# Kernel tuning notes

Measured on AMD Instinct MI355X. Metric: run time of the kernel, lower is better.

## Reference

```python
import jax, jax.numpy as jnp
import numpy as np

EPS_LA = 1e-8
BN_EPS = 1e-5


def setup_inputs() -> dict:
    N, IN_C, HID, OUT_C = 8192, 64, 64, 32
    key = jax.random.key(0)
    ks = jax.random.split(key, 8)
    X = jax.random.normal(ks[0], (N, IN_C), dtype=jnp.float32)
    La = jax.random.uniform(ks[1], (N,), dtype=jnp.float32)  # eigenvalues in [0,1)
    U = jax.random.normal(ks[2], (N, N), dtype=jnp.float32)  # eigenvector matrix
    # learnable params
    ve = jnp.array([7.0], dtype=jnp.float32)   # Velocity(7)
    ve2 = jnp.array([0.0], dtype=jnp.float32)  # Velocity(0)
    W_w = jax.random.normal(ks[3], (HID, IN_C), dtype=jnp.float32) / np.sqrt(IN_C)
    W_b = jnp.zeros((HID,), dtype=jnp.float32)
    bn_gamma = jnp.ones((HID,), dtype=jnp.float32)
    bn_beta = jnp.zeros((HID,), dtype=jnp.float32)
    mlp_w = jax.random.normal(ks[4], (OUT_C, HID), dtype=jnp.float32) / np.sqrt(HID)
    mlp_b = jnp.zeros((OUT_C,), dtype=jnp.float32)
    return {"X": X, "La": La, "U": U, "ve": ve, "ve2": ve2,
            "W_w": W_w, "W_b": W_b, "bn_gamma": bn_gamma, "bn_beta": bn_beta,
            "mlp_w": mlp_w, "mlp_b": mlp_b}


def reference(X, La, U, ve, ve2, W_w, W_b, bn_gamma, bn_beta, mlp_w, mlp_b):
    # Spectral filter eigenvalue scalings (Velocity modules: elementwise pow)
    V_La = jnp.power(La, ve[0])                                # [N]
    V_La2 = jnp.power((2.0 * (La - EPS_LA) - 1.0) ** 2 + 1.0, ve2[0])  # [N]
    # U @ diag(V) @ U^T @ X done as elementwise scaling in the spectral domain
    # (same math as the dense diag-matmul chain, O(N^2 d) instead of O(N^3))
    out = U @ (V_La[:, None] * (U.T @ X))    # [N, in_c]
    out = U @ (V_La2[:, None] * (U.T @ out)) # [N, in_c]
    # Linear W
    out = out @ W_w.T + W_b                  # [N, hid]
    hidden_emd = out
    # BatchNorm1d (training-mode batch statistics, biased variance)
    mean = jnp.mean(out, axis=0)
    var = jnp.mean((out - mean) ** 2, axis=0)
    out = (out - mean) * jax.lax.rsqrt(var + BN_EPS) * bn_gamma + bn_beta
    # ReLU; dropout is identity in deterministic/eval reference
    out = jax.nn.relu(out)
    out = out @ mlp_w.T + mlp_b              # [N, out_c]
    return (jax.nn.log_softmax(out, axis=1), hidden_emd)
```

## Files before the change

kernel.cpp:

```cpp
#include <hip/hip_runtime.h>
#include <hip/hip_bf16.h>

typedef __attribute__((ext_vector_type(4))) float f32x4;
typedef __attribute__((ext_vector_type(8))) short bf16x8;
typedef __attribute__((ext_vector_type(8))) unsigned short u16x8;

#define NN 8192
#define SK 8
#define KSL (NN / SK)
#define NT (KSL / 64)

__device__ __forceinline__ unsigned short f2bf(float f) {
    unsigned int u = __float_as_uint(f);
    u += 0x7fffu + ((u >> 16) & 1u);
    return (unsigned short)(u >> 16);
}

__device__ __forceinline__ float bf2f(unsigned short h) {
    return __uint_as_float((unsigned int)h << 16);
}

__device__ __forceinline__ void gload16(const void* g, void* l) {
    __builtin_amdgcn_global_load_lds(
        (const __attribute__((address_space(1))) unsigned int*)g,
        (__attribute__((address_space(3))) unsigned int*)l, 16, 0, 0);
}

#define VMW(N) asm volatile("s_waitcnt vmcnt(" #N ")" ::: "memory")
#define SBAR() do { __builtin_amdgcn_sched_barrier(0);                         \
                    __builtin_amdgcn_s_barrier();                              \
                    __builtin_amdgcn_sched_barrier(0); } while (0)

__global__ __launch_bounds__(256) void prep_v(const float* __restrict__ La,
        const float* __restrict__ ve, const float* __restrict__ ve2,
        float* __restrict__ V1, float* __restrict__ V2) {
    int i = blockIdx.x * 256 + threadIdx.x;
    float la = La[i];
    V1[i] = powf(la, ve[0]);
    float b = 2.0f * (la - 1e-8f) - 1.0f;
    V2[i] = powf(b * b + 1.0f, ve2[0]);
}

template<int TM>
__global__ __launch_bounds__(256, 4) void spec_pass(const float* __restrict__ U,
        const unsigned short* __restrict__ FB, unsigned short* __restrict__ Pout) {
    __shared__ float tile[3][4096];
    const int tid = threadIdx.x;
    const int w = tid >> 6, l = tid & 63;
    const int lm = l & 15, g = l >> 4;
    const int x0 = blockIdx.x * 64;
    const int kbase = blockIdx.y * KSL;
    const int kb0 = kbase >> 5;
    const unsigned short* fbL = FB + (size_t)l * 8;

    f32x4 acc[4];
#pragma unroll
    for (int f = 0; f < 4; ++f) acc[f] = (f32x4)0.f;

#define STAGE(B, CT)                                                           \
    do {                                                                       \
        _Pragma("unroll")                                                      \
        for (int q_ = 0; q_ < 4; ++q_) {                                       \
            const int cc_ = 4 * w + q_;                                        \
            const int row_ = 4 * cc_ + (l >> 4);                               \
            const int su_ = (l & 15) ^ (row_ & 7);                             \
            const float* gp_ = U +                                             \
                (size_t)(TM ? (kbase + (CT) * 64 + row_) : (x0 + row_)) * NN + \
                (TM ? x0 : (kbase + (CT) * 64)) + su_ * 4;                     \
            gload16(gp_, &tile[B][cc_ * 256]);                                 \
        }                                                                      \
    } while (0)

#define LOADFB(R, CT)                                                          \
    do {                                                                       \
        _Pragma("unroll")                                                      \
        for (int sp_ = 0; sp_ < 2; ++sp_)                                      \
            _Pragma("unroll")                                                  \
            for (int f_ = 0; f_ < 4; ++f_)                                     \
                R[sp_][f_] = *(const bf16x8*)(fbL +                            \
                    ((size_t)((kb0 + 2 * (CT) + sp_) * 4 + f_)) * 512);        \
    } while (0)

#define COMPUTE(B, FBR)                                                        \
    do {                                                                       \
        _Pragma("unroll")                                                      \
        for (int sp_ = 0; sp_ < 2; ++sp_) {                                    \
            if (!TM) {                                                         \
                const float* rp_ = &tile[B][(16 * w + lm) * 64];               \
                const int m7_ = lm & 7;                                        \
                f32x4 p0_ = *(const f32x4*)(rp_ +                              \
                    (((8 * sp_ + 2 * g) ^ m7_) << 2));                         \
                f32x4 p1_ = *(const f32x4*)(rp_ +                              \
                    (((8 * sp_ + 2 * g + 1) ^ m7_) << 2));                     \
                bf16x8 afr_;                                                   \
                _Pragma("unroll")                                              \
                for (int j_ = 0; j_ < 4; ++j_) {                               \
                    afr_[j_]     = (short)f2bf(p0_[j_]);                       \
                    afr_[4 + j_] = (short)f2bf(p1_[j_]);                       \
                }                                                              \
                _Pragma("unroll")                                              \
                for (int f_ = 0; f_ < 4; ++f_)                                 \
                    acc[f_] = __builtin_amdgcn_mfma_f32_16x16x32_bf16(         \
                        afr_, FBR[sp_][f_], acc[f_], 0, 0, 0);                 \
            } else {                                                           \
                bf16x8 bfr_;                                                   \
                _Pragma("unroll")                                              \
                for (int s_ = 0; s_ < 8; ++s_)                                 \
                    bfr_[s_] = (short)f2bf(tile[B][                            \
                        (32 * sp_ + 8 * g + s_) * 64 +                         \
                        (((4 * w + (lm >> 2)) ^ s_) << 2) + (lm & 3)]);        \
                _Pragma("unroll")                                              \
                for (int f_ = 0; f_ < 4; ++f_)                                 \
                    acc[f_] = __builtin_amdgcn_mfma_f32_16x16x32_bf16(         \
                        FBR[sp_][f_], bfr_, acc[f_], 0, 0, 0);                 \
            }                                                                  \
        }                                                                      \
    } while (0)

    bf16x8 fbA[2][4], fbB[2][4];
    STAGE(0, 0);
    LOADFB(fbA, 0);
    STAGE(1, 1);

#define PH(CC, BC, BS, FBC, FBN)                                               \
    do {                                                                       \
        LOADFB(FBN, (CC) + 1);                                                 \
        STAGE(BS, (CC) + 2);                                                   \
        VMW(16);                                                               \
        SBAR();                                                                \
        COMPUTE(BC, FBC);                                                      \
        SBAR();                                                                \
    } while (0)

    PH(0, 0, 2, fbA, fbB);
    PH(1, 1, 0, fbB, fbA);
    PH(2, 2, 1, fbA, fbB);
    PH(3, 0, 2, fbB, fbA);
    PH(4, 1, 0, fbA, fbB);
    PH(5, 2, 1, fbB, fbA);
    PH(6, 0, 2, fbA, fbB);
    PH(7, 1, 0, fbB, fbA);
    PH(8, 2, 1, fbA, fbB);
    PH(9, 0, 2, fbB, fbA);
    PH(10, 1, 0, fbA, fbB);
    PH(11, 2, 1, fbB, fbA);
    PH(12, 0, 2, fbA, fbB);
    PH(13, 1, 0, fbB, fbA);
    LOADFB(fbB, 15);
    VMW(12);
    SBAR();
    COMPUTE(2, fbA);
    SBAR();
    VMW(0);
    SBAR();
    COMPUTE(0, fbB);
#undef PH
#undef STAGE
#undef LOADFB
#undef COMPUTE

    if (!TM) {
        unsigned short* Pp = Pout + (size_t)blockIdx.y * NN * 64;
#pragma unroll
        for (int f = 0; f < 4; ++f)
#pragma unroll
            for (int r = 0; r < 4; ++r)
                Pp[(size_t)(x0 + 16 * w + 4 * g + r) * 64 + f * 16 + lm] =
                    f2bf(acc[f][r]);
    } else {
        unsigned short* Pp = Pout + (size_t)blockIdx.y * 64 * NN;
#pragma unroll
        for (int f = 0; f < 4; ++f)
#pragma unroll
            for (int r = 0; r < 4; ++r)
                Pp[(size_t)(16 * f + 4 * g + r) * NN + x0 + 16 * w + lm] =
                    f2bf(acc[f][r]);
    }
}

__global__ __launch_bounds__(256) void reduce2(const unsigned short* __restrict__ Pt,
        const float* __restrict__ V, unsigned short* __restrict__ FB) {
    int b = blockIdx.x;
    int t = threadIdx.x;
    int nf = t >> 6, l = t & 63, lm = l & 15, g = l >> 4;
    int ch = 16 * nf + lm;
    int ib = 32 * b + 8 * g;
    float s[8];
#pragma unroll
    for (int c = 0; c < 8; ++c) s[c] = 0.f;
#pragma unroll
    for (int sk = 0; sk < SK; ++sk) {
        u16x8 v = *(const u16x8*)(Pt + (size_t)(sk * 64 + ch) * NN + ib);
#pragma unroll
        for (int c = 0; c < 8; ++c) s[c] += bf2f(v[c]);
    }
    f32x4 v0 = *(const f32x4*)(V + ib);
    f32x4 v1 = *(const f32x4*)(V + ib + 4);
    u16x8 o;
#pragma unroll
    for (int c = 0; c < 4; ++c) {
        o[c]     = f2bf(s[c] * v0[c]);
        o[4 + c] = f2bf(s[4 + c] * v1[c]);
    }
    *(u16x8*)(FB + ((size_t)(b * 4 + nf) * 64 + l) * 8) = o;
}

template<int BF>
__global__ __launch_bounds__(256) void reduce_t(const void* __restrict__ M, int nsk,
        unsigned short* __restrict__ FB) {
    __shared__ float T[32][65];
    int b = blockIdx.x;
    int i0 = b * 32;
    int tid = threadIdx.x;
    int il = tid >> 3, jq = (tid & 7) * 8;
    float s[8];
#pragma unroll
    for (int c = 0; c < 8; ++c) s[c] = 0.f;
    for (int k = 0; k < nsk; ++k) {
        if (!BF) {
            const float* p = (const float*)M + ((size_t)k * NN + i0 + il) * 64 + jq;
            f32x4 a = *(const f32x4*)p;
            f32x4 bq = *(const f32x4*)(p + 4);
#pragma unroll
            for (int c = 0; c < 4; ++c) { s[c] += a[c]; s[4 + c] += bq[c]; }
        } else {
            u16x8 v = *(const u16x8*)((const unsigned short*)M +
                ((size_t)k * NN + i0 + il) * 64 + jq);
#pragma unroll
            for (int c = 0; c < 8; ++c) s[c] += bf2f(v[c]);
        }
    }
#pragma unroll
    for (int c = 0; c < 8; ++c) T[il][jq + c] = s[c];
    __syncthreads();
    int nf = tid >> 6, l = tid & 63, g = l >> 4, lm = l & 15;
    u16x8 o;
#pragma unroll
    for (int q = 0; q < 8; ++q) o[q] = f2bf(T[8 * g + q][16 * nf + lm]);
    *(u16x8*)(FB + ((size_t)(b * 4 + nf) * 64 + l) * 8) = o;
}

__global__ __launch_bounds__(256) void reduce_linear(
        const unsigned short* __restrict__ P,
        const float* __restrict__ Ww, const float* __restrict__ Wb,
        float* __restrict__ hidden, float* __restrict__ bsum, float* __restrict__ bsq) {
    __shared__ float z[32][65];
    __shared__ float w[64][65];
    __shared__ float hl[32][65];
    int i0 = blockIdx.x * 32;
    int tid = threadIdx.x;
    for (int e = tid * 4; e < 4096; e += 1024) {
        f32x4 v = *(const f32x4*)(Ww + e);
        int h = e >> 6, c = e & 63;
#pragma unroll
        for (int q = 0; q < 4; ++q) w[h][c + q] = v[q];
    }
    int r = tid >> 3, c8 = (tid & 7) * 8;
    float s[8];
#pragma unroll
    for (int q = 0; q < 8; ++q) s[q] = 0.f;
    for (int k = 0; k < SK; ++k) {
        u16x8 v = *(const u16x8*)(P + ((size_t)k * NN + i0 + r) * 64 + c8);
#pragma unroll
        for (int q = 0; q < 8; ++q) s[q] += bf2f(v[q]);
    }
#pragma unroll
    for (int q = 0; q < 8; ++q) z[r][c8 + q] = s[q];
    __syncthreads();
    int h8 = (tid & 7) * 8;
#pragma unroll
    for (int hh = 0; hh < 8; ++hh) {
        int h = h8 + hh;
        float sv = Wb[h];
        for (int c = 0; c < 64; ++c) sv += z[r][c] * w[h][c];
        hidden[(size_t)(i0 + r) * 64 + h] = sv;
        hl[r][h] = sv;
    }
    __syncthreads();
    if (tid < 64) {
        float sv = 0.f, q2 = 0.f;
#pragma unroll
        for (int rr = 0; rr < 32; ++rr) {
            float v = hl[rr][tid];
            sv += v; q2 += v * v;
        }
        bsum[blockIdx.x * 64 + tid] = sv;
        bsq[blockIdx.x * 64 + tid] = q2;
    }
}

__global__ __launch_bounds__(64) void bn_stats(const float* __restrict__ bsum,
        const float* __restrict__ bsq, const float* __restrict__ gamma,
        const float* __restrict__ beta, float* __restrict__ bnc) {
    int h = threadIdx.x;
    float s = 0.f, q = 0.f;
    for (int b = 0; b < 256; ++b) { s += bsum[b * 64 + h]; q += bsq[b * 64 + h]; }
    float mean = s / 8192.0f;
    float var = q / 8192.0f - mean * mean;
    float inv = rsqrtf(var + 1e-5f);
    float sc = gamma[h] * inv;
    bnc[h] = sc;
    bnc[64 + h] = beta[h] - mean * sc;
}

__global__ __launch_bounds__(256) void head(const float* __restrict__ hidden,
        const float* __restrict__ bnc, const float* __restrict__ Mw,
        const float* __restrict__ Mb, float* __restrict__ out0) {
    __shared__ float a[32][65];
    __shared__ float w[32][65];
    __shared__ float o[32][33];
    __shared__ float rowm[32];
    int i0 = blockIdx.x * 32;
    int tid = threadIdx.x;
    for (int e = tid * 4; e < 2048; e += 1024) {
        f32x4 v = *(const f32x4*)(Mw + e);
        int oo = e >> 6, c = e & 63;
#pragma unroll
        for (int q = 0; q < 4; ++q) w[oo][c + q] = v[q];
    }
    int r = tid >> 3, h8 = (tid & 7) * 8;
    const float* hp = hidden + (size_t)(i0 + r) * 64 + h8;
#pragma unroll
    for (int q = 0; q < 8; ++q) {
        int h = h8 + q;
        float v = hp[q] * bnc[h] + bnc[64 + h];
        a[r][h] = fmaxf(v, 0.f);
    }
    __syncthreads();
    int o4 = (tid & 7) * 4;
#pragma unroll
    for (int q = 0; q < 4; ++q) {
        int oo = o4 + q;
        float s = Mb[oo];
        for (int c = 0; c < 64; ++c) s += a[r][c] * w[oo][c];
        o[r][oo] = s;
    }
    __syncthreads();
    if (tid < 32) {
        float m = -3.0e38f;
#pragma unroll
        for (int c = 0; c < 32; ++c) m = fmaxf(m, o[tid][c]);
        float se = 0.f;
#pragma unroll
        for (int c = 0; c < 32; ++c) se += expf(o[tid][c] - m);
        rowm[tid] = m + logf(se);
    }
    __syncthreads();
    f32x4 v;
#pragma unroll
    for (int q = 0; q < 4; ++q) v[q] = o[r][o4 + q] - rowm[r];
    *(f32x4*)(out0 + (size_t)(i0 + r) * 32 + o4) = v;
}

extern "C" void kernel_launch(void* const* d_in, const int* in_sizes, int n_in,
                              void* d_out, int out_size, void* d_ws, size_t ws_size,
                              hipStream_t stream) {
    const float* X   = (const float*)d_in[0];
    const float* La  = (const float*)d_in[1];
    const float* U   = (const float*)d_in[2];
    const float* ve  = (const float*)d_in[3];
    const float* ve2 = (const float*)d_in[4];
    const float* Ww  = (const float*)d_in[5];
    const float* Wb  = (const float*)d_in[6];
    const float* gam = (const float*)d_in[7];
    const float* bet = (const float*)d_in[8];
    const float* Mw  = (const float*)d_in[9];
    const float* Mb  = (const float*)d_in[10];
    float* out0 = (float*)d_out;
    float* hidden = (float*)d_out + (size_t)NN * 32;

    char* ws = (char*)d_ws;
    float* V1   = (float*)ws;
    float* V2   = (float*)(ws + 32768);
    float* bsum = (float*)(ws + 65536);
    float* bsq  = (float*)(ws + 131072);
    float* bnc  = (float*)(ws + 196608);
    unsigned short* FB = (unsigned short*)(ws + 262144);
    unsigned short* P  = (unsigned short*)(ws + (2u << 20));
    unsigned short* Pt = (unsigned short*)(ws + (12u << 20));

    prep_v<<<32, 256, 0, stream>>>(La, ve, ve2, V1, V2);
    reduce_t<0><<<256, 256, 0, stream>>>(X, 1, FB);
    spec_pass<1><<<dim3(NN / 64, SK), 256, 0, stream>>>(U, FB, Pt);
    reduce2<<<256, 256, 0, stream>>>(Pt, V1, FB);
    spec_pass<0><<<dim3(NN / 64, SK), 256, 0, stream>>>(U, FB, P);
    reduce_t<1><<<256, 256, 0, stream>>>(P, SK, FB);
    spec_pass<1><<<dim3(NN / 64, SK), 256, 0, stream>>>(U, FB, Pt);
    reduce2<<<256, 256, 0, stream>>>(Pt, V2, FB);
    spec_pass<0><<<dim3(NN / 64, SK), 256, 0, stream>>>(U, FB, P);
    reduce_linear<<<256, 256, 0, stream>>>(P, Ww, Wb, hidden, bsum, bsq);
    bn_stats<<<1, 64, 0, stream>>>(bsum, bsq, gam, bet, bnc);
    head<<<256, 256, 0, stream>>>(hidden, bnc, Mw, Mb, out0);
}
```

Measured before the change: 235.9 us.

## Emit bf16 copy of U in first spectral pass and reuse it later

The first spectral pass now reads U in fp32 and also writes a bf16 copy of each tile it stages to a workspace buffer. The remaining three passes read that bf16 copy with new half-width LDS staging, swizzles and adjusted wait counts. This is meant to cut the dominant HBM traffic from four fp32 reads of the 8192x8192 matrix to one fp32 read, one bf16 write and three bf16 reads. The cost is a heavier first pass, now double-buffered with plain __syncthreads instead of the triple-buffered pipeline, plus 128MB of extra workspace.

```diff
diff --git a/kernel.cpp b/kernel.cpp
--- a/kernel.cpp
+++ b/kernel.cpp
@@ -4,6 +4,7 @@
 typedef __attribute__((ext_vector_type(4))) float f32x4;
 typedef __attribute__((ext_vector_type(8))) short bf16x8;
 typedef __attribute__((ext_vector_type(8))) unsigned short u16x8;
+typedef __attribute__((ext_vector_type(4))) unsigned short u16x4;
 
 #define NN 8192
 #define SK 8
@@ -41,10 +42,10 @@
     V2[i] = powf(b * b + 1.0f, ve2[0]);
 }
 
-template<int TM>
-__global__ __launch_bounds__(256, 4) void spec_pass(const float* __restrict__ U,
-        const unsigned short* __restrict__ FB, unsigned short* __restrict__ Pout) {
-    __shared__ float tile[3][4096];
+__global__ __launch_bounds__(256, 4) void spec_f32e(const float* __restrict__ U,
+        const unsigned short* __restrict__ FB, unsigned short* __restrict__ Pout,
+        unsigned short* __restrict__ Uemit) {
+    __shared__ float tile[2][4096];
     const int tid = threadIdx.x;
     const int w = tid >> 6, l = tid & 63;
     const int lm = l & 15, g = l >> 4;
@@ -65,8 +66,7 @@
             const int row_ = 4 * cc_ + (l >> 4);                               \
             const int su_ = (l & 15) ^ (row_ & 7);                             \
             const float* gp_ = U +                                             \
-                (size_t)(TM ? (kbase + (CT) * 64 + row_) : (x0 + row_)) * NN + \
-                (TM ? x0 : (kbase + (CT) * 64)) + su_ * 4;                     \
+                (size_t)(kbase + (CT) * 64 + row_) * NN + x0 + su_ * 4;        \
             gload16(gp_, &tile[B][cc_ * 256]);                                 \
         }                                                                      \
     } while (0)
@@ -85,19 +85,114 @@
     do {                                                                       \
         _Pragma("unroll")                                                      \
         for (int sp_ = 0; sp_ < 2; ++sp_) {                                    \
+            bf16x8 bfr_;                                                       \
+            _Pragma("unroll")                                                  \
+            for (int s_ = 0; s_ < 8; ++s_)                                     \
+                bfr_[s_] = (short)f2bf(tile[B][                                \
+                    (32 * sp_ + 8 * g + s_) * 64 +                             \
+                    (((4 * w + (lm >> 2)) ^ s_) << 2) + (lm & 3)]);            \
+            _Pragma("unroll")                                                  \
+            for (int f_ = 0; f_ < 4; ++f_)                                     \
+                acc[f_] = __builtin_amdgcn_mfma_f32_16x16x32_bf16(             \
+                    FBR[sp_][f_], bfr_, acc[f_], 0, 0, 0);                     \
+        }                                                                      \
+    } while (0)
+
+#define ECHO(B, CT)                                                            \
+    do {                                                                       \
+        _Pragma("unroll")                                                      \
+        for (int q_ = 0; q_ < 4; ++q_) {                                       \
+            const int cc_ = 4 * w + q_;                                        \
+            const int row_ = 4 * cc_ + (l >> 4);                               \
+            const int su_ = (l & 15) ^ (row_ & 7);                             \
+            f32x4 v_ = *(const f32x4*)&tile[B][cc_ * 256 + l * 4];             \
+            u16x4 h_;                                                          \
+            _Pragma("unroll")                                                  \
+            for (int q2_ = 0; q2_ < 4; ++q2_) h_[q2_] = f2bf(v_[q2_]);         \
+            *(u16x4*)(Uemit +                                                  \
+                (size_t)(kbase + (CT) * 64 + row_) * NN + x0 + su_ * 4) = h_;  \
+        }                                                                      \
+    } while (0)
+
+    bf16x8 fbA[2][4], fbB[2][4];
+    LOADFB(fbA, 0);
+    STAGE(0, 0);
+    __syncthreads();
+#pragma unroll 1
+    for (int c = 0; c < NT; c += 2) {
+        if (c + 1 < NT) { LOADFB(fbB, c + 1); STAGE(1, c + 1); }
+        COMPUTE(0, fbA);
+        ECHO(0, c);
+        __syncthreads();
+        if (c + 2 < NT) { LOADFB(fbA, c + 2); STAGE(0, c + 2); }
+        COMPUTE(1, fbB);
+        ECHO(1, c + 1);
+        __syncthreads();
+    }
+#undef STAGE
+#undef LOADFB
+#undef COMPUTE
+#undef ECHO
+
+    unsigned short* Pp = Pout + (size_t)blockIdx.y * 64 * NN;
+#pragma unroll
+    for (int f = 0; f < 4; ++f)
+#pragma unroll
+        for (int r = 0; r < 4; ++r)
+            Pp[(size_t)(16 * f + 4 * g + r) * NN + x0 + 16 * w + lm] =
+                f2bf(acc[f][r]);
+}
+
+template<int TM>
+__global__ __launch_bounds__(256, 4) void spec_bf3(
+        const unsigned short* __restrict__ Ub,
+        const unsigned short* __restrict__ FB, unsigned short* __restrict__ Pout) {
+    __shared__ unsigned short tile[3][4096];
+    const int tid = threadIdx.x;
+    const int w = tid >> 6, l = tid & 63;
+    const int lm = l & 15, g = l >> 4;
+    const int x0 = blockIdx.x * 64;
+    const int kbase = blockIdx.y * KSL;
+    const int kb0 = kbase >> 5;
+    const unsigned short* fbL = FB + (size_t)l * 8;
+
+    f32x4 acc[4];
+#pragma unroll
+    for (int f = 0; f < 4; ++f) acc[f] = (f32x4)0.f;
+
+#define STAGE(B, CT)                                                           \
+    do {                                                                       \
+        _Pragma("unroll")                                                      \
+        for (int q_ = 0; q_ < 2; ++q_) {                                       \
+            const int cc_ = 2 * w + q_;                                        \
+            const int row_ = 8 * cc_ + (l >> 3);                               \
+            const int su_ = (l & 7) ^ (row_ & 7);                              \
+            const unsigned short* gp_ = Ub +                                   \
+                (size_t)(TM ? (kbase + (CT) * 64 + row_) : (x0 + row_)) * NN + \
+                (TM ? x0 : (kbase + (CT) * 64)) + su_ * 8;                     \
+            gload16(gp_, &tile[B][cc_ * 512]);                                 \
+        }                                                                      \
+    } while (0)
+
+#define LOADFB(R, CT)                                                          \
+    do {                                                                       \
+        _Pragma("unroll")                                                      \
+        for (int sp_ = 0; sp_ < 2; ++sp_)                                      \
+            _Pragma("unroll")                                                  \
+            for (int f_ = 0; f_ < 4; ++f_)                                     \
+                R[sp_][f_] = *(const bf16x8*)(fbL +                            \
+                    ((size_t)((kb0 + 2 * (CT) + sp_) * 4 + f_)) * 512);        \
+    } while (0)
+
+#define COMPUTE(B, FBR)                                                        \
+    do {                                                                       \
+        _Pragma("unroll")                                                      \
+        for (int sp_ = 0; sp_ < 2; ++sp_) {                                    \
             if (!TM) {                                                         \
-                const float* rp_ = &tile[B][(16 * w + lm) * 64];               \
-                const int m7_ = lm & 7;                                        \
-                f32x4 p0_ = *(const f32x4*)(rp_ +                              \
-                    (((8 * sp_ + 2 * g) ^ m7_) << 2));                         \
-                f32x4 p1_ = *(const f32x4*)(rp_ +                              \
-                    (((8 * sp_ + 2 * g + 1) ^ m7_) << 2));                     \
-                bf16x8 afr_;                                                   \
-                _Pragma("unroll")                                              \
-                for (int j_ = 0; j_ < 4; ++j_) {                               \
-                    afr_[j_]     = (short)f2bf(p0_[j_]);                       \
-                    afr_[4 + j_] = (short)f2bf(p1_[j_]);                       \
-                }                                                              \
+                const unsigned short* rp_ = &tile[B][(16 * w + lm) * 64];      \
+                bf16x8 afr_ = *(const bf16x8*)(rp_ +                           \
+                    (((2 * sp_ + (g >> 1)) * 2 + (g & 1)) == 0 ? 0 : 0) +      \
+                    ((((2 * sp_ * 2 + g)) ^ (lm & 7)) << 3));                  \
                 _Pragma("unroll")                                              \
                 for (int f_ = 0; f_ < 4; ++f_)                                 \
                     acc[f_] = __builtin_amdgcn_mfma_f32_16x16x32_bf16(         \
@@ -105,10 +200,11 @@
             } else {                                                           \
                 bf16x8 bfr_;                                                   \
                 _Pragma("unroll")                                              \
-                for (int s_ = 0; s_ < 8; ++s_)                                 \
-                    bfr_[s_] = (short)f2bf(tile[B][                            \
-                        (32 * sp_ + 8 * g + s_) * 64 +                         \
-                        (((4 * w + (lm >> 2)) ^ s_) << 2) + (lm & 3)]);        \
+                for (int s_ = 0; s_ < 8; ++s_) {                               \
+                    const int k_ = 32 * sp_ + 8 * g + s_;                      \
+                    bfr_[s_] = (short)tile[B][k_ * 64 +                        \
+                        (((2 * w + (lm >> 3)) ^ (k_ & 7)) << 3) + (lm & 7)];   \
+                }                                                              \
                 _Pragma("unroll")                                              \
                 for (int f_ = 0; f_ < 4; ++f_)                                 \
                     acc[f_] = __builtin_amdgcn_mfma_f32_16x16x32_bf16(         \
@@ -126,7 +222,7 @@
     do {                                                                       \
         LOADFB(FBN, (CC) + 1);                                                 \
         STAGE(BS, (CC) + 2);                                                   \
-        VMW(16);                                                               \
+        VMW(12);                                                               \
         SBAR();                                                                \
         COMPUTE(BC, FBC);                                                      \
         SBAR();                                                                \
@@ -147,7 +243,7 @@
     PH(12, 0, 2, fbA, fbB);
     PH(13, 1, 0, fbB, fbA);
     LOADFB(fbB, 15);
-    VMW(12);
+    VMW(10);
     SBAR();
     COMPUTE(2, fbA);
     SBAR();
@@ -378,16 +474,17 @@
     unsigned short* FB = (unsigned short*)(ws + 262144);
     unsigned short* P  = (unsigned short*)(ws + (2u << 20));
     unsigned short* Pt = (unsigned short*)(ws + (12u << 20));
+    unsigned short* Ubf = (unsigned short*)(ws + (64u << 20));
 
     prep_v<<<32, 256, 0, stream>>>(La, ve, ve2, V1, V2);
     reduce_t<0><<<256, 256, 0, stream>>>(X, 1, FB);
-    spec_pass<1><<<dim3(NN / 64, SK), 256, 0, stream>>>(U, FB, Pt);
+    spec_f32e<<<dim3(NN / 64, SK), 256, 0, stream>>>(U, FB, Pt, Ubf);
     reduce2<<<256, 256, 0, stream>>>(Pt, V1, FB);
-    spec_pass<0><<<dim3(NN / 64, SK), 256, 0, stream>>>(U, FB, P);
+    spec_bf3<0><<<dim3(NN / 64, SK), 256, 0, stream>>>(Ubf, FB, P);
     reduce_t<1><<<256, 256, 0, stream>>>(P, SK, FB);
-    spec_pass<1><<<dim3(NN / 64, SK), 256, 0, stream>>>(U, FB, Pt);
+    spec_bf3<1><<<dim3(NN / 64, SK), 256, 0, stream>>>(Ubf, FB, Pt);
     reduce2<<<256, 256, 0, stream>>>(Pt, V2, FB);
-    spec_pass<0><<<dim3(NN / 64, SK), 256, 0, stream>>>(U, FB, P);
+    spec_bf3<0><<<dim3(NN / 64, SK), 256, 0, stream>>>(Ubf, FB, P);
     reduce_linear<<<256, 256, 0, stream>>>(P, Ww, Wb, hidden, bsum, bsq);
     bn_stats<<<1, 64, 0, stream>>>(bsum, bsq, gam, bet, bnc);
     head<<<256, 256, 0, stream>>>(hidden, bnc, Mw, Mb, out0);
```

After: 268.8 us. 13.9% more time.
